# Kernel tuning notes

Hardware: AMD Instinct MI355X
Metric: run time of the kernel (lower is better)

Reference implementation:

```python
import jax, jax.numpy as jnp
import numpy as np

W = 32        # local_context
M = 128       # nb_features
TEMP = 1.0    # softmax_temp
NEG = -1e24   # mask fill used by local_dot_product in the original


def _log_features(x, proj):
    # Performer softmax-kernel log-features (before stabilization).
    # x: (B,H,N,E), proj: (M,E) -> (B,H,N,M); exp(q.k*TEMP) ~ (1/M) sum_m phi_q phi_k
    xn = x * np.float32(np.sqrt(TEMP))
    d = jnp.einsum('bhne,me->bhnm', xn, proj)
    diag = 0.5 * jnp.sum(xn * xn, axis=-1, keepdims=True)
    return d - diag


def _sb_local_chunk(q, k, v, proj):
    # Scatterbrain SBLocalAttention: exact softmax scores inside a centered local
    # window of size W, Performer low-rank approximation outside, shared normalizer.
    # q: (B,H,L,E) chunk queries; k,v: (B,H,S,E); proj: (M,E)
    B, H, L, E = q.shape
    S = k.shape[2]
    nb, half = L // W, W // 2

    logq = _log_features(q, proj)
    stab_q = jax.lax.stop_gradient(jnp.max(logq, axis=-1, keepdims=True))        # per-query stabilizer
    phi_q = jnp.exp(logq - stab_q)
    logk = _log_features(k, proj)
    stab_k = jax.lax.stop_gradient(jnp.max(logk, axis=(-1, -2), keepdims=True))  # global key stabilizer
    phi_k = jnp.exp(logk - stab_k)
    # true low-rank score = (phi_q . phi_k) * exp(prime_log_scale)
    pls = stab_q[..., 0] + stab_k[..., 0] - np.float32(np.log(M))                # (B,H,L)

    # Low-rank (linear attention) sums over ALL keys
    kv = jnp.einsum('bhsm,bhsd->bhmd', phi_k, v)
    lr_v = jnp.einsum('bhlm,bhmd->bhld', phi_q, kv)            # (B,H,L,E)
    lr_1 = jnp.einsum('bhlm,bhm->bhl', phi_q, phi_k.sum(2))    # (B,H,L)

    # Local window: query position t attends keys [t-W//2, t+W//2).
    # Gather 3 key blocks of size W per query block instead of per-query windows.
    q_blk = q.reshape(B, H, nb, W, E)
    phiq_blk = phi_q.reshape(B, H, nb, W, M)
    idx3 = W * jnp.arange(nb)[:, None] + jnp.arange(3 * W)[None, :]   # (nb,3W) into padded seq
    pad = [(0, 0), (0, 0), (W, W), (0, 0)]
    k3 = jnp.pad(k, pad)[:, :, idx3]          # (B,H,nb,3W,E)
    v3 = jnp.pad(v, pad)[:, :, idx3]
    phik3 = jnp.pad(phi_k, pad)[:, :, idx3]   # (B,H,nb,3W,M)

    pos = idx3[:, None, :] - W                # absolute key positions (nb,1,3W)
    rel = pos - (W * jnp.arange(nb)[:, None, None] + jnp.arange(W)[None, :, None])
    mask = (rel >= -half) & (rel < half) & (pos >= 0) & (pos < S)     # (nb,W,3W)

    scores = TEMP * jnp.einsum('bhnqe,bhnke->bhnqk', q_blk, k3)
    scores = jnp.where(mask, scores, NEG)
    dots_p = jnp.where(mask, jnp.einsum('bhnqm,bhnkm->bhnqk', phiq_blk, phik3), 0.0)

    qk_lse = jax.nn.logsumexp(scores, axis=-1).reshape(B, H, L)
    # low-rank mass minus the in-window part it double counts (>= 0 since phi >= 0)
    lr_rem = jnp.clip(lr_1 - dots_p.sum(-1).reshape(B, H, L), 1e-24, None)
    log_norm = jnp.logaddexp(qk_lse, jnp.log(lr_rem) + pls)           # (B,H,L)

    p_local = jnp.exp(scores - log_norm.reshape(B, H, nb, W, 1))
    out_local = jnp.einsum('bhnqk,bhnke->bhnqe', p_local, v3).reshape(B, H, L, E)
    lr_v_win = jnp.einsum('bhnqk,bhnke->bhnqe', dots_p, v3).reshape(B, H, L, E)
    return out_local + (lr_v - lr_v_win) * jnp.exp(pls - log_norm)[..., None]


def _forward(query, key, value, proj):
    # query/key/value: (B,T,H,E) as in the torch module; proj: (4,M,E), one random
    # feature matrix per chunk (module builds a fresh SBLocalAttention each chunk).
    q = jnp.transpose(query, (0, 2, 1, 3))
    k = jnp.transpose(key, (0, 2, 1, 3))
    v = jnp.transpose(value, (0, 2, 1, 3))
    B, H, T, E = q.shape
    CH = 1024
    qc = q.reshape(B, H, T // CH, CH, E).transpose(2, 0, 1, 3, 4)     # (4,B,H,CH,E)
    outs = jax.vmap(_sb_local_chunk, in_axes=(0, None, None, 0))(qc, k, v, proj)
    # torch.cat(att, 1).transpose(1, 2) -> (B,H,T,E)
    return outs.transpose(1, 2, 0, 3, 4).reshape(B, H, T, E)


def setup_inputs() -> dict:
    key = jax.random.key(0)
    k1, k2, k3, k4 = jax.random.split(key, 4)
    B, T, S, H, E = 4, 4096, 4096, 8, 64
    return {
        'query': jax.random.normal(k1, (B, T, H, E), dtype=jnp.float32),
        'key': jax.random.normal(k2, (B, S, H, E), dtype=jnp.float32),
        'value': jax.random.normal(k3, (B, S, H, E), dtype=jnp.float32),
        'proj': jax.random.normal(k4, (4, M, E), dtype=jnp.float32),
    }


def reference(query, key, value, proj):
    return _forward(query, key, value, proj)
```

## Files before the change

### kernel.cpp

```cpp
#include <hip/hip_runtime.h>

typedef unsigned short u16;
typedef unsigned int   u32;
typedef __attribute__((ext_vector_type(8))) short short8;
typedef __attribute__((ext_vector_type(4))) float f32x4;

#define LOGM 4.852030263919617f

constexpr int WS_PMAX = 0;
constexpr int WS_K1   = 2048;
constexpr int WS_KV   = 18432;
constexpr int WS_PHIK = 1067008;
constexpr int WS_PLS  = 9717760;
constexpr int WS_LR1  = 9848832;
constexpr int WS_PHIQ = 9979904;
constexpr int WS_LRV  = 18368512;

__device__ __forceinline__ float b2f(u16 u){ union { u32 i; float f; } x; x.i = ((u32)u) << 16; return x.f; }
__device__ __forceinline__ u16 f2b(float f){ union { float f; u32 i; } x; x.f = f; return (u16)((x.i + 0x7fffu + ((x.i >> 16) & 1u)) >> 16); }

__global__ __launch_bounds__(256, 2) void k_phi(const float* __restrict__ key,
                                                const float* __restrict__ val,
                                                const float* __restrict__ proj,
                                                float* __restrict__ ws){
  __shared__ __align__(16) u16 phit[128*72];
  __shared__ __align__(16) u16 vt[64*72];
  __shared__ float sred[4];
  const int tid = threadIdx.x;
  const int wave = tid >> 6, l = tid & 63;
  const int g = l >> 4, r16 = l & 15;
  const int kq = blockIdx.x, combo = blockIdx.y;
  const int c = combo >> 5, b = (combo >> 3) & 3, h = combo & 7;
  const float* projc = proj + c*8192;

  {
    const float4* pr = (const float4*)(projc + (tid & 127)*64);
    float pn = 0.f;
    #pragma unroll
    for(int i=0;i<16;i++){ float4 u = pr[i]; pn = fmaf(u.x,u.x,fmaf(u.y,u.y,fmaf(u.z,u.z,fmaf(u.w,u.w,pn)))); }
    #pragma unroll
    for(int o=1;o<64;o<<=1) pn = fmaxf(pn, __shfl_xor(pn, o));
    if(l == 0) sred[wave] = pn;
  }
  __syncthreads();
  const float stab = 0.5f * fmaxf(fmaxf(sred[0],sred[1]), fmaxf(sred[2],sred[3]));
  if(kq == 0 && tid == 0) ws[WS_PMAX + combo] = stab;

  short8 ph[8][2], pl[8][2];
  #pragma unroll
  for(int mt=0;mt<8;mt++){
    #pragma unroll
    for(int ks=0;ks<2;ks++){
      const float* pb = projc + (mt*16 + r16)*64 + ks*32 + g*8;
      float4 u0 = *(const float4*)pb;
      float4 u1 = *(const float4*)(pb + 4);
      float x[8] = {u0.x,u0.y,u0.z,u0.w,u1.x,u1.y,u1.z,u1.w};
      #pragma unroll
      for(int j=0;j<8;j++){
        u16 hb = f2b(x[j]);
        ph[mt][ks][j] = (short)hb;
        pl[mt][ks][j] = (short)f2b(x[j] - b2f(hb));
      }
    }
  }

  const f32x4 zero4 = {0.f,0.f,0.f,0.f};
  f32x4 kvacc[2][4];
  #pragma unroll
  for(int i=0;i<2;i++)
    #pragma unroll
    for(int j=0;j<4;j++) kvacc[i][j] = zero4;
  float k1p0 = 0.f, k1p1 = 0.f;
  u16* phikg = ((u16*)(ws + WS_PHIK)) + (size_t)combo*1056*128;

  for(int t0=0;t0<16;t0++){
    const int s_tile = kq*1024 + t0*64;
    const int sA = s_tile + wave*16 + r16;
    const float* krow = key + (size_t)(b*4096 + sA)*512 + h*64;
    float areg[16];
    #pragma unroll
    for(int ks=0;ks<2;ks++){
      float4 u0 = *(const float4*)(krow + ks*32 + g*8);
      float4 u1 = *(const float4*)(krow + ks*32 + g*8 + 4);
      areg[ks*8+0]=u0.x; areg[ks*8+1]=u0.y; areg[ks*8+2]=u0.z; areg[ks*8+3]=u0.w;
      areg[ks*8+4]=u1.x; areg[ks*8+5]=u1.y; areg[ks*8+6]=u1.z; areg[ks*8+7]=u1.w;
    }
    float ksq = 0.f;
    #pragma unroll
    for(int e=0;e<16;e++) ksq = fmaf(areg[e], areg[e], ksq);
    ksq += __shfl_xor(ksq, 16);
    ksq += __shfl_xor(ksq, 32);
    ksq *= 0.5f;
    short8 ah[2], al[2];
    #pragma unroll
    for(int ks=0;ks<2;ks++){
      #pragma unroll
      for(int j=0;j<8;j++){
        float x = areg[ks*8+j];
        u16 hb = f2b(x);
        ah[ks][j] = (short)hb;
        al[ks][j] = (short)f2b(x - b2f(hb));
      }
    }
    f32x4 acc[8];
    #pragma unroll
    for(int mt=0;mt<8;mt++) acc[mt] = zero4;
    #pragma unroll
    for(int ks=0;ks<2;ks++){
      #pragma unroll
      for(int mt=0;mt<8;mt++){
        acc[mt] = __builtin_amdgcn_mfma_f32_16x16x32_bf16(ah[ks], ph[mt][ks], acc[mt], 0, 0, 0);
        acc[mt] = __builtin_amdgcn_mfma_f32_16x16x32_bf16(ah[ks], pl[mt][ks], acc[mt], 0, 0, 0);
        acc[mt] = __builtin_amdgcn_mfma_f32_16x16x32_bf16(al[ks], ph[mt][ks], acc[mt], 0, 0, 0);
      }
    }
    const float kc0 = __shfl(ksq, 4*g + 0);
    const float kc1 = __shfl(ksq, 4*g + 1);
    const float kc2 = __shfl(ksq, 4*g + 2);
    const float kc3 = __shfl(ksq, 4*g + 3);
    #pragma unroll
    for(int mt=0;mt<8;mt++){
      ushort4 pw;
      pw.x = f2b(__expf(acc[mt][0] - kc0 - stab));
      pw.y = f2b(__expf(acc[mt][1] - kc1 - stab));
      pw.z = f2b(__expf(acc[mt][2] - kc2 - stab));
      pw.w = f2b(__expf(acc[mt][3] - kc3 - stab));
      *(ushort4*)(phit + (mt*16 + r16)*72 + wave*16 + 4*g) = pw;
    }
    __syncthreads();
    if(s_tile < 1056){
      const int m = tid & 127, kh = tid >> 7;
      for(int kk=0;kk<32;kk++){
        int skey = kh*32 + kk, gs = s_tile + skey;
        if(gs < 1056) phikg[(size_t)gs*128 + m] = phit[m*72 + skey];
      }
    }
    #pragma unroll
    for(int i=0;i<4;i++){
      int flat = tid + 256*i;
      int sv = flat >> 4, d4 = (flat & 15)*4;
      const float4 u = *(const float4*)(val + (size_t)(b*4096 + s_tile + sv)*512 + h*64 + d4);
      vt[(d4+0)*72 + sv] = f2b(u.x);
      vt[(d4+1)*72 + sv] = f2b(u.y);
      vt[(d4+2)*72 + sv] = f2b(u.z);
      vt[(d4+3)*72 + sv] = f2b(u.w);
    }
    __syncthreads();
    #pragma unroll
    for(int ks=0;ks<2;ks++){
      short8 af0 = *(const short8*)(phit + ((2*wave+0)*16 + r16)*72 + ks*32 + g*8);
      short8 af1 = *(const short8*)(phit + ((2*wave+1)*16 + r16)*72 + ks*32 + g*8);
      short8 bf[4];
      #pragma unroll
      for(int dt=0;dt<4;dt++) bf[dt] = *(const short8*)(vt + (dt*16 + r16)*72 + ks*32 + g*8);
      #pragma unroll
      for(int dt=0;dt<4;dt++){
        kvacc[0][dt] = __builtin_amdgcn_mfma_f32_16x16x32_bf16(af0, bf[dt], kvacc[0][dt], 0, 0, 0);
        kvacc[1][dt] = __builtin_amdgcn_mfma_f32_16x16x32_bf16(af1, bf[dt], kvacc[1][dt], 0, 0, 0);
      }
      #pragma unroll
      for(int j=0;j<8;j++){ k1p0 += b2f((u16)af0[j]); k1p1 += b2f((u16)af1[j]); }
    }
    __syncthreads();
  }
  k1p0 += __shfl_xor(k1p0, 16); k1p0 += __shfl_xor(k1p0, 32);
  k1p1 += __shfl_xor(k1p1, 16); k1p1 += __shfl_xor(k1p1, 32);
  if(l < 16){
    atomicAdd(ws + WS_K1 + combo*128 + (2*wave+0)*16 + l, k1p0);
    atomicAdd(ws + WS_K1 + combo*128 + (2*wave+1)*16 + l, k1p1);
  }
  #pragma unroll
  for(int mi=0;mi<2;mi++){
    #pragma unroll
    for(int dt=0;dt<4;dt++){
      #pragma unroll
      for(int rr=0;rr<4;rr++){
        int m = (2*wave+mi)*16 + 4*g + rr;
        int d = dt*16 + r16;
        atomicAdd(ws + WS_KV + (size_t)combo*8192 + m*64 + d, kvacc[mi][dt][rr]);
      }
    }
  }
}

__global__ __launch_bounds__(256, 2) void k_q(const float* __restrict__ qry,
                                              const float* __restrict__ proj,
                                              float* __restrict__ ws){
  __shared__ __align__(16) u16 phiqs[64*136];
  __shared__ __align__(16) u16 kvt[64*136];
  __shared__ float k1s[128];
  const int tid = threadIdx.x;
  const int wave = tid >> 6, l = tid & 63;
  const int g = l >> 4, r16 = l & 15;
  const int qt = blockIdx.x, combo = blockIdx.y;
  const int c = combo >> 5, b = (combo >> 3) & 3, h = combo & 7;
  const float* projc = proj + c*8192;
  const float stab = ws[WS_PMAX + combo];
  if(tid < 128) k1s[tid] = ws[WS_K1 + combo*128 + tid];
  const float* kvg = ws + WS_KV + (size_t)combo*8192;
  #pragma unroll
  for(int i=0;i<8;i++){
    int flat = tid + 256*i;
    int m = flat >> 4, d4 = (flat & 15)*4;
    float4 u = *(const float4*)(kvg + m*64 + d4);
    kvt[(d4+0)*136 + m] = f2b(u.x);
    kvt[(d4+1)*136 + m] = f2b(u.y);
    kvt[(d4+2)*136 + m] = f2b(u.z);
    kvt[(d4+3)*136 + m] = f2b(u.w);
  }
  const int qrow = qt*64 + wave*16 + r16;
  const float* qr = qry + (size_t)(b*4096 + (c*1024 + qrow))*512 + h*64;
  float areg[16];
  #pragma unroll
  for(int ks=0;ks<2;ks++){
    float4 u0 = *(const float4*)(qr + ks*32 + g*8);
    float4 u1 = *(const float4*)(qr + ks*32 + g*8 + 4);
    areg[ks*8+0]=u0.x; areg[ks*8+1]=u0.y; areg[ks*8+2]=u0.z; areg[ks*8+3]=u0.w;
    areg[ks*8+4]=u1.x; areg[ks*8+5]=u1.y; areg[ks*8+6]=u1.z; areg[ks*8+7]=u1.w;
  }
  float qsq = 0.f;
  #pragma unroll
  for(int e=0;e<16;e++) qsq = fmaf(areg[e], areg[e], qsq);
  qsq += __shfl_xor(qsq, 16);
  qsq += __shfl_xor(qsq, 32);
  qsq *= 0.5f;
  short8 ah[2], al[2];
  #pragma unroll
  for(int ks=0;ks<2;ks++){
    #pragma unroll
    for(int j=0;j<8;j++){
      float x = areg[ks*8+j];
      u16 hb = f2b(x);
      ah[ks][j] = (short)hb;
      al[ks][j] = (short)f2b(x - b2f(hb));
    }
  }
  const f32x4 zero4 = {0.f,0.f,0.f,0.f};
  f32x4 acc[8];
  #pragma unroll
  for(int mt=0;mt<8;mt++) acc[mt] = zero4;
  #pragma unroll
  for(int ks=0;ks<2;ks++){
    #pragma unroll
    for(int mt=0;mt<8;mt++){
      const float* pb = projc + (mt*16 + r16)*64 + ks*32 + g*8;
      float4 u0 = *(const float4*)pb;
      float4 u1 = *(const float4*)(pb + 4);
      float x[8] = {u0.x,u0.y,u0.z,u0.w,u1.x,u1.y,u1.z,u1.w};
      short8 pph, ppl;
      #pragma unroll
      for(int j=0;j<8;j++){
        u16 hb = f2b(x[j]);
        pph[j] = (short)hb;
        ppl[j] = (short)f2b(x[j] - b2f(hb));
      }
      acc[mt] = __builtin_amdgcn_mfma_f32_16x16x32_bf16(ah[ks], pph, acc[mt], 0, 0, 0);
      acc[mt] = __builtin_amdgcn_mfma_f32_16x16x32_bf16(ah[ks], ppl, acc[mt], 0, 0, 0);
      acc[mt] = __builtin_amdgcn_mfma_f32_16x16x32_bf16(al[ks], pph, acc[mt], 0, 0, 0);
    }
  }
  float qsr[4];
  #pragma unroll
  for(int r=0;r<4;r++) qsr[r] = __shfl(qsq, 4*g + r);
  float amax[4];
  #pragma unroll
  for(int r=0;r<4;r++){
    float m = -3e38f;
    #pragma unroll
    for(int mt=0;mt<8;mt++) m = fmaxf(m, acc[mt][r]);
    m = fmaxf(m, __shfl_xor(m, 1));
    m = fmaxf(m, __shfl_xor(m, 2));
    m = fmaxf(m, __shfl_xor(m, 4));
    m = fmaxf(m, __shfl_xor(m, 8));
    amax[r] = m;
  }
  float lrp[4] = {0.f,0.f,0.f,0.f};
  #pragma unroll
  for(int mt=0;mt<8;mt++){
    const float k1v = k1s[mt*16 + r16];
    #pragma unroll
    for(int r=0;r<4;r++){
      float phv = __expf(acc[mt][r] - amax[r]);
      phiqs[(wave*16 + 4*g + r)*136 + mt*16 + r16] = f2b(phv);
      lrp[r] = fmaf(phv, k1v, lrp[r]);
    }
  }
  #pragma unroll
  for(int r=0;r<4;r++){
    lrp[r] += __shfl_xor(lrp[r], 1);
    lrp[r] += __shfl_xor(lrp[r], 2);
    lrp[r] += __shfl_xor(lrp[r], 4);
    lrp[r] += __shfl_xor(lrp[r], 8);
  }
  if(r16 == 0){
    #pragma unroll
    for(int r=0;r<4;r++){
      int row = qt*64 + wave*16 + 4*g + r;
      ws[WS_PLS + combo*1024 + row] = amax[r] - qsr[r] + stab - LOGM;
      ws[WS_LR1 + combo*1024 + row] = lrp[r];
    }
  }
  __syncthreads();
  f32x4 lacc[4];
  #pragma unroll
  for(int dt=0;dt<4;dt++) lacc[dt] = zero4;
  #pragma unroll
  for(int ks=0;ks<4;ks++){
    short8 a = *(const short8*)(phiqs + (wave*16 + r16)*136 + ks*32 + g*8);
    #pragma unroll
    for(int dt=0;dt<4;dt++){
      short8 bfr = *(const short8*)(kvt + (dt*16 + r16)*136 + ks*32 + g*8);
      lacc[dt] = __builtin_amdgcn_mfma_f32_16x16x32_bf16(a, bfr, lacc[dt], 0, 0, 0);
    }
  }
  u16* lrvg = ((u16*)(ws + WS_LRV)) + ((size_t)combo*1024 + qt*64)*64;
  #pragma unroll
  for(int dt=0;dt<4;dt++){
    #pragma unroll
    for(int r=0;r<4;r++)
      lrvg[(wave*16 + 4*g + r)*64 + dt*16 + r16] = f2b(lacc[dt][r]);
  }
  u16* phiqg = ((u16*)(ws + WS_PHIQ)) + ((size_t)combo*1024 + qt*64)*128;
  #pragma unroll
  for(int i=0;i<8;i++){
    int flat = tid + 256*i;
    int row = flat >> 5, c4 = (flat & 31)*4;
    *(ushort4*)(phiqg + flat*4) = *(const ushort4*)(phiqs + row*136 + c4);
  }
}

__global__ __launch_bounds__(256, 2) void k_main(const float* __restrict__ qry,
                                                 const float* __restrict__ key,
                                                 const float* __restrict__ val,
                                                 float* __restrict__ ws,
                                                 float* __restrict__ out){
  __shared__ __align__(16) u16 buf[30720];
  u16* khs  = buf;
  u16* kls  = buf + 6912;
  u16* phik = buf + 13824;
  u16* cjh  = buf;
  u16* cjl  = buf + 8704;
  u16* vt   = buf + 17408;
  u16* vtl  = buf + 24064;

  const int tid = threadIdx.x;
  const int wave = tid >> 6, l = tid & 63;
  const int g = l >> 4, r16 = l & 15;
  const int qt = blockIdx.x, combo = blockIdx.y;
  const int c = combo >> 5, b = (combo >> 3) & 3, h = combo & 7;
  const int s_base = qt*64 - 16;

  const u16* phikg = ((const u16*)(ws + WS_PHIK)) + (size_t)combo*1056*128;
  float4 vreg[6];
  #pragma unroll
  for(int i=0;i<6;i++){
    int flat = tid + 256*i;
    int j = flat >> 4, e4 = (flat & 15)*4;
    int s = s_base + j;
    float4 u = {0.f,0.f,0.f,0.f};
    float4 w4 = {0.f,0.f,0.f,0.f};
    if(s >= 0){
      u  = *(const float4*)(key + (((size_t)b*4096 + s)*8 + h)*64 + e4);
      w4 = *(const float4*)(val + (((size_t)b*4096 + s)*8 + h)*64 + e4);
    }
    vreg[i] = w4;
    ushort4 hh, ll;
    hh.x = f2b(u.x); ll.x = f2b(u.x - b2f(hh.x));
    hh.y = f2b(u.y); ll.y = f2b(u.y - b2f(hh.y));
    hh.z = f2b(u.z); ll.z = f2b(u.z - b2f(hh.z));
    hh.w = f2b(u.w); ll.w = f2b(u.w - b2f(hh.w));
    *(ushort4*)(khs + j*72 + e4) = hh;
    *(ushort4*)(kls + j*72 + e4) = ll;
  }
  #pragma unroll
  for(int i=0;i<12;i++){
    int flat = tid + 256*i;
    int j = flat >> 5, c4 = (flat & 31)*4;
    int s = s_base + j;
    ushort4 p = {0,0,0,0};
    if(s >= 0) p = *(const ushort4*)(phikg + (size_t)s*128 + c4);
    *(ushort4*)(phik + j*136 + c4) = p;
  }
  const int qrow = qt*64 + wave*16 + r16;
  const float* qr = qry + (((size_t)b*4096 + (c*1024 + qrow))*8 + h)*64;
  short8 ah[2], al[2];
  #pragma unroll
  for(int ks=0;ks<2;ks++){
    float4 u0 = *(const float4*)(qr + ks*32 + g*8);
    float4 u1 = *(const float4*)(qr + ks*32 + g*8 + 4);
    float x[8] = {u0.x,u0.y,u0.z,u0.w,u1.x,u1.y,u1.z,u1.w};
    #pragma unroll
    for(int jj=0;jj<8;jj++){
      u16 hb = f2b(x[jj]);
      ah[ks][jj] = (short)hb;
      al[ks][jj] = (short)f2b(x[jj] - b2f(hb));
    }
  }
  const u16* phiqg = ((const u16*)(ws + WS_PHIQ)) + ((size_t)combo*1024 + qt*64)*128;
  short8 pa[4];
  #pragma unroll
  for(int ks=0;ks<4;ks++)
    pa[ks] = *(const short8*)(phiqg + (wave*16 + r16)*128 + ks*32 + g*8);
  float plsr[4], lr1r[4];
  #pragma unroll
  for(int r=0;r<4;r++){
    int row = qt*64 + wave*16 + 4*g + r;
    plsr[r] = ws[WS_PLS + combo*1024 + row];
    lr1r[r] = ws[WS_LR1 + combo*1024 + row];
  }
  __syncthreads();

  const f32x4 zero4 = {0.f,0.f,0.f,0.f};
  f32x4 sacc[6], dacc[6];
  #pragma unroll
  for(int j=0;j<6;j++){ sacc[j] = zero4; dacc[j] = zero4; }
  #pragma unroll
  for(int j=0;j<6;j++){
    #pragma unroll
    for(int ks=0;ks<2;ks++){
      short8 kbh = *(const short8*)(khs + (j*16 + r16)*72 + ks*32 + g*8);
      short8 kbl = *(const short8*)(kls + (j*16 + r16)*72 + ks*32 + g*8);
      sacc[j] = __builtin_amdgcn_mfma_f32_16x16x32_bf16(ah[ks], kbh, sacc[j], 0, 0, 0);
      sacc[j] = __builtin_amdgcn_mfma_f32_16x16x32_bf16(al[ks], kbh, sacc[j], 0, 0, 0);
      sacc[j] = __builtin_amdgcn_mfma_f32_16x16x32_bf16(ah[ks], kbl, sacc[j], 0, 0, 0);
    }
    #pragma unroll
    for(int ks=0;ks<4;ks++){
      short8 pb = *(const short8*)(phik + (j*16 + r16)*136 + ks*32 + g*8);
      dacc[j] = __builtin_amdgcn_mfma_f32_16x16x32_bf16(pa[ks], pb, dacc[j], 0, 0, 0);
    }
  }
  __syncthreads();

  #pragma unroll
  for(int i=0;i<6;i++){
    int flat = tid + 256*i;
    int j = flat >> 4, e4 = (flat & 15)*4;
    float4 u = vreg[i];
    u16 h0 = f2b(u.x), h1 = f2b(u.y), h2 = f2b(u.z), h3 = f2b(u.w);
    vt[(e4+0)*104 + j] = h0; vtl[(e4+0)*104 + j] = f2b(u.x - b2f(h0));
    vt[(e4+1)*104 + j] = h1; vtl[(e4+1)*104 + j] = f2b(u.y - b2f(h1));
    vt[(e4+2)*104 + j] = h2; vtl[(e4+2)*104 + j] = f2b(u.z - b2f(h2));
    vt[(e4+3)*104 + j] = h3; vtl[(e4+3)*104 + j] = f2b(u.w - b2f(h3));
  }
  const int rowb = wave*16 + 4*g;
  float m1r[4] = {-1e30f,-1e30f,-1e30f,-1e30f};
  #pragma unroll
  for(int j=0;j<6;j++){
    #pragma unroll
    for(int r=0;r<4;r++){
      int rel = 16*j + r16 - 16 - (rowb + r);
      bool ok = (rel >= -16) && (rel < 16) && (s_base + 16*j + r16 >= 0);
      if(ok) m1r[r] = fmaxf(m1r[r], sacc[j][r]);
    }
  }
  #pragma unroll
  for(int r=0;r<4;r++){
    m1r[r] = fmaxf(m1r[r], __shfl_xor(m1r[r], 1));
    m1r[r] = fmaxf(m1r[r], __shfl_xor(m1r[r], 2));
    m1r[r] = fmaxf(m1r[r], __shfl_xor(m1r[r], 4));
    m1r[r] = fmaxf(m1r[r], __shfl_xor(m1r[r], 8));
  }
  float ser[4] = {0.f,0.f,0.f,0.f}, wpr[4] = {0.f,0.f,0.f,0.f};
  #pragma unroll
  for(int j=0;j<6;j++){
    #pragma unroll
    for(int r=0;r<4;r++){
      int rel = 16*j + r16 - 16 - (rowb + r);
      bool ok = (rel >= -16) && (rel < 16) && (s_base + 16*j + r16 >= 0);
      if(ok){
        ser[r] += __expf(sacc[j][r] - m1r[r]);
        wpr[r] += dacc[j][r];
      }
    }
  }
  #pragma unroll
  for(int r=0;r<4;r++){
    ser[r] += __shfl_xor(ser[r], 1); ser[r] += __shfl_xor(ser[r], 2);
    ser[r] += __shfl_xor(ser[r], 4); ser[r] += __shfl_xor(ser[r], 8);
    wpr[r] += __shfl_xor(wpr[r], 1); wpr[r] += __shfl_xor(wpr[r], 2);
    wpr[r] += __shfl_xor(wpr[r], 4); wpr[r] += __shfl_xor(wpr[r], 8);
  }
  float lnr[4], scr[4];
  #pragma unroll
  for(int r=0;r<4;r++){
    float qk_lse = m1r[r] + __logf(ser[r]);
    float lrem = fmaxf(lr1r[r] - wpr[r], 1e-37f);
    float bb = __logf(lrem) + plsr[r];
    float ln = fmaxf(qk_lse, bb) + log1pf(__expf(-fabsf(qk_lse - bb)));
    lnr[r] = ln;
    scr[r] = __expf(plsr[r] - ln);
  }
  #pragma unroll
  for(int j=0;j<6;j++){
    #pragma unroll
    for(int r=0;r<4;r++){
      int rel = 16*j + r16 - 16 - (rowb + r);
      bool ok = (rel >= -16) && (rel < 16) && (s_base + 16*j + r16 >= 0);
      float cj = ok ? (__expf(sacc[j][r] - lnr[r]) - scr[r]*dacc[j][r]) : 0.f;
      u16 hb = f2b(cj);
      cjh[(rowb + r)*136 + 16*j + r16] = hb;
      cjl[(rowb + r)*136 + 16*j + r16] = f2b(cj - b2f(hb));
    }
  }
  __syncthreads();

  f32x4 oacc[4];
  #pragma unroll
  for(int dt=0;dt<4;dt++) oacc[dt] = zero4;
  #pragma unroll
  for(int ks=0;ks<3;ks++){
    short8 ch = *(const short8*)(cjh + (wave*16 + r16)*136 + ks*32 + g*8);
    short8 cl = *(const short8*)(cjl + (wave*16 + r16)*136 + ks*32 + g*8);
    #pragma unroll
    for(int dt=0;dt<4;dt++){
      short8 vbh = *(const short8*)(vt  + (dt*16 + r16)*104 + ks*32 + g*8);
      short8 vbl = *(const short8*)(vtl + (dt*16 + r16)*104 + ks*32 + g*8);
      oacc[dt] = __builtin_amdgcn_mfma_f32_16x16x32_bf16(ch, vbh, oacc[dt], 0, 0, 0);
      oacc[dt] = __builtin_amdgcn_mfma_f32_16x16x32_bf16(cl, vbh, oacc[dt], 0, 0, 0);
      oacc[dt] = __builtin_amdgcn_mfma_f32_16x16x32_bf16(ch, vbl, oacc[dt], 0, 0, 0);
    }
  }
  const u16* lrvg = ((const u16*)(ws + WS_LRV)) + ((size_t)combo*1024 + qt*64)*64;
  #pragma unroll
  for(int r=0;r<4;r++){
    int row = rowb + r;
    float* ob = out + ((((size_t)b*8 + h)*4096) + (size_t)c*1024 + qt*64 + row)*64;
    #pragma unroll
    for(int dt=0;dt<4;dt++){
      float lv = b2f(lrvg[row*64 + dt*16 + r16]);
      ob[dt*16 + r16] = oacc[dt][r] + scr[r]*lv;
    }
  }
}

extern "C" void kernel_launch(void* const* d_in, const int* in_sizes, int n_in,
                              void* d_out, int out_size, void* d_ws, size_t ws_size,
                              hipStream_t stream){
  (void)in_sizes; (void)n_in; (void)out_size; (void)ws_size;
  const float* q = (const float*)d_in[0];
  const float* k = (const float*)d_in[1];
  const float* v = (const float*)d_in[2];
  const float* p = (const float*)d_in[3];
  float* out = (float*)d_out;
  float* ws = (float*)d_ws;
  hipMemsetAsync(ws + WS_K1, 0, (size_t)(16384 + 1048576)*sizeof(float), stream);
  k_phi <<<dim3(4,128),  256, 0, stream>>>(k, v, p, ws);
  k_q   <<<dim3(16,128), 256, 0, stream>>>(q, p, ws);
  k_main<<<dim3(16,128), 256, 0, stream>>>(q, k, v, ws, out);
}
```

Measured before the change: 370.2 us.

## Split key phase across more blocks with partial buffers and a reduction kernel

The key-feature kernel now uses 8 blocks per head/chunk over 512 keys each instead of 4 over 1024, doubling the grid. Per-block KV and key-sum partials go to separate workspace slots, and a new reduction kernel sums them, replacing the global atomics and the memset. The phi_k store for the first 1056 keys now goes through an LDS transpose buffer and vectorised row writes instead of scalar strided stores. This adds an extra kernel launch and extra partial-buffer traffic. It also reuses the phi_q and lr_v workspace regions as scratch before the later kernels overwrite them.

```diff
diff --git a/kernel.cpp b/kernel.cpp
--- a/kernel.cpp
+++ b/kernel.cpp
@@ -15,6 +15,8 @@
 constexpr int WS_LR1  = 9848832;
 constexpr int WS_PHIQ = 9979904;
 constexpr int WS_LRV  = 18368512;
+constexpr int WS_KVP  = WS_PHIQ;
+constexpr int WS_K1P  = WS_LRV;
 
 __device__ __forceinline__ float b2f(u16 u){ union { u32 i; float f; } x; x.i = ((u32)u) << 16; return x.f; }
 __device__ __forceinline__ u16 f2b(float f){ union { float f; u32 i; } x; x.f = f; return (u16)((x.i + 0x7fffu + ((x.i >> 16) & 1u)) >> 16); }
@@ -24,8 +26,10 @@
                                                 const float* __restrict__ proj,
                                                 float* __restrict__ ws){
   __shared__ __align__(16) u16 phit[128*72];
-  __shared__ __align__(16) u16 vt[64*72];
+  __shared__ __align__(16) u16 buf2[8704];
   __shared__ float sred[4];
+  u16* vt = buf2;
+  u16* phit2 = buf2;
   const int tid = threadIdx.x;
   const int wave = tid >> 6, l = tid & 63;
   const int g = l >> 4, r16 = l & 15;
@@ -73,8 +77,9 @@
   float k1p0 = 0.f, k1p1 = 0.f;
   u16* phikg = ((u16*)(ws + WS_PHIK)) + (size_t)combo*1056*128;
 
-  for(int t0=0;t0<16;t0++){
-    const int s_tile = kq*1024 + t0*64;
+  for(int t0=0;t0<8;t0++){
+    const int s_tile = kq*512 + t0*64;
+    const bool dtile = (s_tile < 1056);
     const int sA = s_tile + wave*16 + r16;
     const float* krow = key + (size_t)(b*4096 + sA)*512 + h*64;
     float areg[16];
@@ -126,14 +131,25 @@
       pw.z = f2b(__expf(acc[mt][2] - kc2 - stab));
       pw.w = f2b(__expf(acc[mt][3] - kc3 - stab));
       *(ushort4*)(phit + (mt*16 + r16)*72 + wave*16 + 4*g) = pw;
+      if(dtile){
+        u16* p2 = phit2 + (wave*16 + 4*g)*132 + mt*16 + r16;
+        p2[0*132] = pw.x;
+        p2[1*132] = pw.y;
+        p2[2*132] = pw.z;
+        p2[3*132] = pw.w;
+      }
     }
     __syncthreads();
-    if(s_tile < 1056){
-      const int m = tid & 127, kh = tid >> 7;
-      for(int kk=0;kk<32;kk++){
-        int skey = kh*32 + kk, gs = s_tile + skey;
-        if(gs < 1056) phikg[(size_t)gs*128 + m] = phit[m*72 + skey];
-      }
+    if(dtile){
+      #pragma unroll
+      for(int i=0;i<8;i++){
+        int flat = tid + 256*i;
+        int row = flat >> 5, c4 = (flat & 31)*4;
+        int gs = s_tile + row;
+        if(gs < 1056)
+          *(ushort4*)(phikg + (size_t)gs*128 + c4) = *(const ushort4*)(phit2 + row*132 + c4);
+      }
+      __syncthreads();
     }
     #pragma unroll
     for(int i=0;i<4;i++){
@@ -166,9 +182,10 @@
   k1p0 += __shfl_xor(k1p0, 16); k1p0 += __shfl_xor(k1p0, 32);
   k1p1 += __shfl_xor(k1p1, 16); k1p1 += __shfl_xor(k1p1, 32);
   if(l < 16){
-    atomicAdd(ws + WS_K1 + combo*128 + (2*wave+0)*16 + l, k1p0);
-    atomicAdd(ws + WS_K1 + combo*128 + (2*wave+1)*16 + l, k1p1);
-  }
+    ws[WS_K1P + kq*16384 + combo*128 + (2*wave+0)*16 + l] = k1p0;
+    ws[WS_K1P + kq*16384 + combo*128 + (2*wave+1)*16 + l] = k1p1;
+  }
+  float* kvp = ws + WS_KVP + (size_t)kq*1048576 + (size_t)combo*8192;
   #pragma unroll
   for(int mi=0;mi<2;mi++){
     #pragma unroll
@@ -177,9 +194,31 @@
       for(int rr=0;rr<4;rr++){
         int m = (2*wave+mi)*16 + 4*g + rr;
         int d = dt*16 + r16;
-        atomicAdd(ws + WS_KV + (size_t)combo*8192 + m*64 + d, kvacc[mi][dt][rr]);
-      }
-    }
+        kvp[m*64 + d] = kvacc[mi][dt][rr];
+      }
+    }
+  }
+}
+
+__global__ __launch_bounds__(256) void k_red(float* __restrict__ ws){
+  const int i = blockIdx.x*256 + threadIdx.x;
+  const float* src = ws + WS_KVP + (size_t)i*4;
+  float4 s = {0.f,0.f,0.f,0.f};
+  #pragma unroll
+  for(int p=0;p<8;p++){
+    float4 u = *(const float4*)(src + (size_t)p*1048576);
+    s.x += u.x; s.y += u.y; s.z += u.z; s.w += u.w;
+  }
+  *(float4*)(ws + WS_KV + (size_t)i*4) = s;
+  if(blockIdx.x < 16){
+    const int j = blockIdx.x*256 + threadIdx.x;
+    float4 t = {0.f,0.f,0.f,0.f};
+    #pragma unroll
+    for(int p=0;p<8;p++){
+      float4 u = *(const float4*)(ws + WS_K1P + p*16384 + j*4);
+      t.x += u.x; t.y += u.y; t.z += u.z; t.w += u.w;
+    }
+    *(float4*)(ws + WS_K1 + j*4) = t;
   }
 }
 
@@ -544,8 +583,8 @@
   const float* p = (const float*)d_in[3];
   float* out = (float*)d_out;
   float* ws = (float*)d_ws;
-  hipMemsetAsync(ws + WS_K1, 0, (size_t)(16384 + 1048576)*sizeof(float), stream);
-  k_phi <<<dim3(4,128),  256, 0, stream>>>(k, v, p, ws);
+  k_phi <<<dim3(8,128),  256, 0, stream>>>(k, v, p, ws);
+  k_red <<<dim3(1024),   256, 0, stream>>>(ws);
   k_q   <<<dim3(16,128), 256, 0, stream>>>(q, p, ws);
   k_main<<<dim3(16,128), 256, 0, stream>>>(q, k, v, ws, out);
 }
```

After: 409.7 us. 1.11x slower.

## Split k_phi over more blocks, prefetch values, swizzle LDS, write phi_k directly

Applied to the files above, without the earlier changes.

Doubles the k_phi grid so each block processes 512 keys instead of 1024, which raises parallelism from 512 to 1024 blocks. Value loads are issued early into registers so they overlap the feature MFMA work. The transposed value tile in LDS uses an XOR swizzle to cut bank conflicts. The phi_k slice for the first 1056 keys is now written straight from registers, which removes a sync and a serial copy loop. More blocks also means more atomicAdd contention on the shared KV and k1 accumulators.

```diff
diff --git a/kernel.cpp b/kernel.cpp
--- a/kernel.cpp
+++ b/kernel.cpp
@@ -73,8 +73,9 @@
   float k1p0 = 0.f, k1p1 = 0.f;
   u16* phikg = ((u16*)(ws + WS_PHIK)) + (size_t)combo*1056*128;
 
-  for(int t0=0;t0<16;t0++){
-    const int s_tile = kq*1024 + t0*64;
+  for(int t0=0;t0<8;t0++){
+    const int s_tile = kq*512 + t0*64;
+    const bool dtile = (s_tile < 1056);
     const int sA = s_tile + wave*16 + r16;
     const float* krow = key + (size_t)(b*4096 + sA)*512 + h*64;
     float areg[16];
@@ -85,6 +86,13 @@
       areg[ks*8+0]=u0.x; areg[ks*8+1]=u0.y; areg[ks*8+2]=u0.z; areg[ks*8+3]=u0.w;
       areg[ks*8+4]=u1.x; areg[ks*8+5]=u1.y; areg[ks*8+6]=u1.z; areg[ks*8+7]=u1.w;
     }
+    float4 vreg[4];
+    #pragma unroll
+    for(int i=0;i<4;i++){
+      int flat = tid + 256*i;
+      int sv = flat >> 4, d4 = (flat & 15)*4;
+      vreg[i] = *(const float4*)(val + (size_t)(b*4096 + s_tile + sv)*512 + h*64 + d4);
+    }
     float ksq = 0.f;
     #pragma unroll
     for(int e=0;e<16;e++) ksq = fmaf(areg[e], areg[e], ksq);
@@ -118,6 +126,7 @@
     const float kc1 = __shfl(ksq, 4*g + 1);
     const float kc2 = __shfl(ksq, 4*g + 2);
     const float kc3 = __shfl(ksq, 4*g + 3);
+    const int gs = s_tile + wave*16 + r16;
     #pragma unroll
     for(int mt=0;mt<8;mt++){
       ushort4 pw;
@@ -126,24 +135,19 @@
       pw.z = f2b(__expf(acc[mt][2] - kc2 - stab));
       pw.w = f2b(__expf(acc[mt][3] - kc3 - stab));
       *(ushort4*)(phit + (mt*16 + r16)*72 + wave*16 + 4*g) = pw;
-    }
-    __syncthreads();
-    if(s_tile < 1056){
-      const int m = tid & 127, kh = tid >> 7;
-      for(int kk=0;kk<32;kk++){
-        int skey = kh*32 + kk, gs = s_tile + skey;
-        if(gs < 1056) phikg[(size_t)gs*128 + m] = phit[m*72 + skey];
-      }
+      if(dtile && gs < 1056)
+        *(ushort4*)(phikg + (size_t)gs*128 + mt*16 + 4*g) = pw;
     }
     #pragma unroll
     for(int i=0;i<4;i++){
       int flat = tid + 256*i;
       int sv = flat >> 4, d4 = (flat & 15)*4;
-      const float4 u = *(const float4*)(val + (size_t)(b*4096 + s_tile + sv)*512 + h*64 + d4);
-      vt[(d4+0)*72 + sv] = f2b(u.x);
-      vt[(d4+1)*72 + sv] = f2b(u.y);
-      vt[(d4+2)*72 + sv] = f2b(u.z);
-      vt[(d4+3)*72 + sv] = f2b(u.w);
+      float x[4] = {vreg[i].x, vreg[i].y, vreg[i].z, vreg[i].w};
+      #pragma unroll
+      for(int j=0;j<4;j++){
+        int d = d4 + j;
+        vt[d*72 + (sv ^ (8*((d>>2)&7)))] = f2b(x[j]);
+      }
     }
     __syncthreads();
     #pragma unroll
@@ -152,7 +156,11 @@
       short8 af1 = *(const short8*)(phit + ((2*wave+1)*16 + r16)*72 + ks*32 + g*8);
       short8 bf[4];
       #pragma unroll
-      for(int dt=0;dt<4;dt++) bf[dt] = *(const short8*)(vt + (dt*16 + r16)*72 + ks*32 + g*8);
+      for(int dt=0;dt<4;dt++){
+        int d = dt*16 + r16;
+        int col = (ks*32 + g*8) ^ (8*((d>>2)&7));
+        bf[dt] = *(const short8*)(vt + d*72 + col);
+      }
       #pragma unroll
       for(int dt=0;dt<4;dt++){
         kvacc[0][dt] = __builtin_amdgcn_mfma_f32_16x16x32_bf16(af0, bf[dt], kvacc[0][dt], 0, 0, 0);
@@ -545,7 +553,7 @@
   float* out = (float*)d_out;
   float* ws = (float*)d_ws;
   hipMemsetAsync(ws + WS_K1, 0, (size_t)(16384 + 1048576)*sizeof(float), stream);
-  k_phi <<<dim3(4,128),  256, 0, stream>>>(k, v, p, ws);
+  k_phi <<<dim3(8,128),  256, 0, stream>>>(k, v, p, ws);
   k_q   <<<dim3(16,128), 256, 0, stream>>>(q, p, ws);
   k_main<<<dim3(16,128), 256, 0, stream>>>(q, k, v, ws, out);
 }
```

New measurement: 408.2 us. 10.2% more time.

## Double-buffer phi/V tiles in k_phi, prefetch keys, swizzle V LDS

Applied to the files above, without the earlier changes.

Restructures the k_phi tile loop to use double-buffered LDS for phi and V, which removes one of the two barriers per tile. Key rows for the next tile are prefetched into registers, and value loads are issued early. The phi_k global write now goes straight from registers instead of through a serial LDS copy loop. V is stored transposed with an XOR swizzle to cut LDS bank conflicts. Register pressure goes up, which may hurt occupancy under the 2-blocks launch bound.

```diff
diff --git a/kernel.cpp b/kernel.cpp
--- a/kernel.cpp
+++ b/kernel.cpp
@@ -23,8 +23,8 @@
                                                 const float* __restrict__ val,
                                                 const float* __restrict__ proj,
                                                 float* __restrict__ ws){
-  __shared__ __align__(16) u16 phit[128*72];
-  __shared__ __align__(16) u16 vt[64*72];
+  __shared__ __align__(16) u16 phit[2][128*72];
+  __shared__ __align__(16) u16 vt[2][64*72];
   __shared__ float sred[4];
   const int tid = threadIdx.x;
   const int wave = tid >> 6, l = tid & 63;
@@ -32,6 +32,15 @@
   const int kq = blockIdx.x, combo = blockIdx.y;
   const int c = combo >> 5, b = (combo >> 3) & 3, h = combo & 7;
   const float* projc = proj + c*8192;
+
+  float4 ka[4], kb[4];
+  {
+    const float* krow0 = key + (size_t)(b*4096 + kq*1024 + wave*16 + r16)*512 + h*64;
+    ka[0] = *(const float4*)(krow0 + g*8);
+    ka[1] = *(const float4*)(krow0 + g*8 + 4);
+    ka[2] = *(const float4*)(krow0 + 32 + g*8);
+    ka[3] = *(const float4*)(krow0 + 32 + g*8 + 4);
+  }
 
   {
     const float4* pr = (const float4*)(projc + (tid & 127)*64);
@@ -73,96 +82,108 @@
   float k1p0 = 0.f, k1p1 = 0.f;
   u16* phikg = ((u16*)(ws + WS_PHIK)) + (size_t)combo*1056*128;
 
-  for(int t0=0;t0<16;t0++){
-    const int s_tile = kq*1024 + t0*64;
-    const int sA = s_tile + wave*16 + r16;
-    const float* krow = key + (size_t)(b*4096 + sA)*512 + h*64;
-    float areg[16];
-    #pragma unroll
-    for(int ks=0;ks<2;ks++){
-      float4 u0 = *(const float4*)(krow + ks*32 + g*8);
-      float4 u1 = *(const float4*)(krow + ks*32 + g*8 + 4);
-      areg[ks*8+0]=u0.x; areg[ks*8+1]=u0.y; areg[ks*8+2]=u0.z; areg[ks*8+3]=u0.w;
-      areg[ks*8+4]=u1.x; areg[ks*8+5]=u1.y; areg[ks*8+6]=u1.z; areg[ks*8+7]=u1.w;
-    }
-    float ksq = 0.f;
-    #pragma unroll
-    for(int e=0;e<16;e++) ksq = fmaf(areg[e], areg[e], ksq);
-    ksq += __shfl_xor(ksq, 16);
-    ksq += __shfl_xor(ksq, 32);
-    ksq *= 0.5f;
-    short8 ah[2], al[2];
-    #pragma unroll
-    for(int ks=0;ks<2;ks++){
-      #pragma unroll
-      for(int j=0;j<8;j++){
-        float x = areg[ks*8+j];
-        u16 hb = f2b(x);
-        ah[ks][j] = (short)hb;
-        al[ks][j] = (short)f2b(x - b2f(hb));
-      }
-    }
-    f32x4 acc[8];
-    #pragma unroll
-    for(int mt=0;mt<8;mt++) acc[mt] = zero4;
-    #pragma unroll
-    for(int ks=0;ks<2;ks++){
-      #pragma unroll
-      for(int mt=0;mt<8;mt++){
-        acc[mt] = __builtin_amdgcn_mfma_f32_16x16x32_bf16(ah[ks], ph[mt][ks], acc[mt], 0, 0, 0);
-        acc[mt] = __builtin_amdgcn_mfma_f32_16x16x32_bf16(ah[ks], pl[mt][ks], acc[mt], 0, 0, 0);
-        acc[mt] = __builtin_amdgcn_mfma_f32_16x16x32_bf16(al[ks], ph[mt][ks], acc[mt], 0, 0, 0);
-      }
-    }
-    const float kc0 = __shfl(ksq, 4*g + 0);
-    const float kc1 = __shfl(ksq, 4*g + 1);
-    const float kc2 = __shfl(ksq, 4*g + 2);
-    const float kc3 = __shfl(ksq, 4*g + 3);
-    #pragma unroll
-    for(int mt=0;mt<8;mt++){
-      ushort4 pw;
-      pw.x = f2b(__expf(acc[mt][0] - kc0 - stab));
-      pw.y = f2b(__expf(acc[mt][1] - kc1 - stab));
-      pw.z = f2b(__expf(acc[mt][2] - kc2 - stab));
-      pw.w = f2b(__expf(acc[mt][3] - kc3 - stab));
-      *(ushort4*)(phit + (mt*16 + r16)*72 + wave*16 + 4*g) = pw;
-    }
-    __syncthreads();
-    if(s_tile < 1056){
-      const int m = tid & 127, kh = tid >> 7;
-      for(int kk=0;kk<32;kk++){
-        int skey = kh*32 + kk, gs = s_tile + skey;
-        if(gs < 1056) phikg[(size_t)gs*128 + m] = phit[m*72 + skey];
-      }
-    }
-    #pragma unroll
-    for(int i=0;i<4;i++){
-      int flat = tid + 256*i;
-      int sv = flat >> 4, d4 = (flat & 15)*4;
-      const float4 u = *(const float4*)(val + (size_t)(b*4096 + s_tile + sv)*512 + h*64 + d4);
-      vt[(d4+0)*72 + sv] = f2b(u.x);
-      vt[(d4+1)*72 + sv] = f2b(u.y);
-      vt[(d4+2)*72 + sv] = f2b(u.z);
-      vt[(d4+3)*72 + sv] = f2b(u.w);
-    }
-    __syncthreads();
-    #pragma unroll
-    for(int ks=0;ks<2;ks++){
-      short8 af0 = *(const short8*)(phit + ((2*wave+0)*16 + r16)*72 + ks*32 + g*8);
-      short8 af1 = *(const short8*)(phit + ((2*wave+1)*16 + r16)*72 + ks*32 + g*8);
-      short8 bf[4];
-      #pragma unroll
-      for(int dt=0;dt<4;dt++) bf[dt] = *(const short8*)(vt + (dt*16 + r16)*72 + ks*32 + g*8);
-      #pragma unroll
-      for(int dt=0;dt<4;dt++){
-        kvacc[0][dt] = __builtin_amdgcn_mfma_f32_16x16x32_bf16(af0, bf[dt], kvacc[0][dt], 0, 0, 0);
-        kvacc[1][dt] = __builtin_amdgcn_mfma_f32_16x16x32_bf16(af1, bf[dt], kvacc[1][dt], 0, 0, 0);
-      }
-      #pragma unroll
-      for(int j=0;j<8;j++){ k1p0 += b2f((u16)af0[j]); k1p1 += b2f((u16)af1[j]); }
-    }
-    __syncthreads();
-  }
+#define PHI_TILE(T0, KC, KN, PB)                                                          \
+{                                                                                          \
+  const int s_tile = kq*1024 + (T0)*64;                                                    \
+  const bool dtile = (s_tile < 1056);                                                      \
+  if((T0) < 15){                                                                           \
+    const float* krow2 = key + (size_t)(b*4096 + s_tile + 64 + wave*16 + r16)*512 + h*64;  \
+    KN[0] = *(const float4*)(krow2 + g*8);                                                 \
+    KN[1] = *(const float4*)(krow2 + g*8 + 4);                                             \
+    KN[2] = *(const float4*)(krow2 + 32 + g*8);                                            \
+    KN[3] = *(const float4*)(krow2 + 32 + g*8 + 4);                                        \
+  }                                                                                        \
+  float4 vreg[4];                                                                          \
+  _Pragma("unroll")                                                                        \
+  for(int i=0;i<4;i++){                                                                    \
+    int flat = tid + 256*i;                                                                \
+    int sv = flat >> 4, d4 = (flat & 15)*4;                                                \
+    vreg[i] = *(const float4*)(val + (size_t)(b*4096 + s_tile + sv)*512 + h*64 + d4);      \
+  }                                                                                        \
+  float areg[16] = {KC[0].x,KC[0].y,KC[0].z,KC[0].w, KC[1].x,KC[1].y,KC[1].z,KC[1].w,      \
+                    KC[2].x,KC[2].y,KC[2].z,KC[2].w, KC[3].x,KC[3].y,KC[3].z,KC[3].w};     \
+  float ksq = 0.f;                                                                         \
+  _Pragma("unroll")                                                                        \
+  for(int e=0;e<16;e++) ksq = fmaf(areg[e], areg[e], ksq);                                 \
+  ksq += __shfl_xor(ksq, 16); ksq += __shfl_xor(ksq, 32); ksq *= 0.5f;                     \
+  short8 ah[2], al[2];                                                                     \
+  _Pragma("unroll")                                                                        \
+  for(int ks=0;ks<2;ks++){                                                                 \
+    _Pragma("unroll")                                                                      \
+    for(int j=0;j<8;j++){                                                                  \
+      float x = areg[ks*8+j];                                                              \
+      u16 hb = f2b(x);                                                                     \
+      ah[ks][j] = (short)hb;                                                               \
+      al[ks][j] = (short)f2b(x - b2f(hb));                                                 \
+    }                                                                                      \
+  }                                                                                        \
+  f32x4 acc[8];                                                                            \
+  _Pragma("unroll")                                                                        \
+  for(int mt=0;mt<8;mt++) acc[mt] = zero4;                                                 \
+  _Pragma("unroll")                                                                        \
+  for(int ks=0;ks<2;ks++){                                                                 \
+    _Pragma("unroll")                                                                      \
+    for(int mt=0;mt<8;mt++){                                                               \
+      acc[mt] = __builtin_amdgcn_mfma_f32_16x16x32_bf16(ah[ks], ph[mt][ks], acc[mt],0,0,0);\
+      acc[mt] = __builtin_amdgcn_mfma_f32_16x16x32_bf16(ah[ks], pl[mt][ks], acc[mt],0,0,0);\
+      acc[mt] = __builtin_amdgcn_mfma_f32_16x16x32_bf16(al[ks], ph[mt][ks], acc[mt],0,0,0);\
+    }                                                                                      \
+  }                                                                                        \
+  const float kc0 = __shfl(ksq, 4*g + 0);                                                  \
+  const float kc1 = __shfl(ksq, 4*g + 1);                                                  \
+  const float kc2 = __shfl(ksq, 4*g + 2);                                                  \
+  const float kc3 = __shfl(ksq, 4*g + 3);                                                  \
+  const int gs = s_tile + wave*16 + r16;                                                   \
+  _Pragma("unroll")                                                                        \
+  for(int mt=0;mt<8;mt++){                                                                 \
+    ushort4 pw;                                                                            \
+    pw.x = f2b(__expf(acc[mt][0] - kc0 - stab));                                           \
+    pw.y = f2b(__expf(acc[mt][1] - kc1 - stab));                                           \
+    pw.z = f2b(__expf(acc[mt][2] - kc2 - stab));                                           \
+    pw.w = f2b(__expf(acc[mt][3] - kc3 - stab));                                           \
+    *(ushort4*)(phit[PB] + (mt*16 + r16)*72 + wave*16 + 4*g) = pw;                         \
+    if(dtile && gs < 1056)                                                                 \
+      *(ushort4*)(phikg + (size_t)gs*128 + mt*16 + 4*g) = pw;                              \
+  }                                                                                        \
+  _Pragma("unroll")                                                                        \
+  for(int i=0;i<4;i++){                                                                    \
+    int flat = tid + 256*i;                                                                \
+    int sv = flat >> 4, d4 = (flat & 15)*4;                                                \
+    float xx[4] = {vreg[i].x, vreg[i].y, vreg[i].z, vreg[i].w};                            \
+    _Pragma("unroll")                                                                      \
+    for(int j=0;j<4;j++){                                                                  \
+      int d = d4 + j;                                                                      \
+      vt[PB][d*72 + (sv ^ (8*((d>>2)&7)))] = f2b(xx[j]);                                   \
+    }                                                                                      \
+  }                                                                                        \
+  __syncthreads();                                                                         \
+  _Pragma("unroll")                                                                        \
+  for(int ks=0;ks<2;ks++){                                                                 \
+    short8 af0 = *(const short8*)(phit[PB] + ((2*wave+0)*16 + r16)*72 + ks*32 + g*8);      \
+    short8 af1 = *(const short8*)(phit[PB] + ((2*wave+1)*16 + r16)*72 + ks*32 + g*8);      \
+    short8 bfv[4];                                                                         \
+    _Pragma("unroll")                                                                      \
+    for(int dt=0;dt<4;dt++){                                                               \
+      int d = dt*16 + r16;                                                                 \
+      int col = (ks*32 + g*8) ^ (8*((d>>2)&7));                                            \
+      bfv[dt] = *(const short8*)(vt[PB] + d*72 + col);                                     \
+    }                                                                                      \
+    _Pragma("unroll")                                                                      \
+    for(int dt=0;dt<4;dt++){                                                               \
+      kvacc[0][dt] = __builtin_amdgcn_mfma_f32_16x16x32_bf16(af0, bfv[dt], kvacc[0][dt],0,0,0); \
+      kvacc[1][dt] = __builtin_amdgcn_mfma_f32_16x16x32_bf16(af1, bfv[dt], kvacc[1][dt],0,0,0); \
+    }                                                                                      \
+    _Pragma("unroll")                                                                      \
+    for(int j=0;j<8;j++){ k1p0 += b2f((u16)af0[j]); k1p1 += b2f((u16)af1[j]); }            \
+  }                                                                                        \
+}
+
+  for(int tt=0; tt<16; tt+=2){
+    PHI_TILE(tt,   ka, kb, 0)
+    PHI_TILE(tt+1, kb, ka, 1)
+  }
+#undef PHI_TILE
+
   k1p0 += __shfl_xor(k1p0, 16); k1p0 += __shfl_xor(k1p0, 32);
   k1p1 += __shfl_xor(k1p1, 16); k1p1 += __shfl_xor(k1p1, 32);
   if(l < 16){
```

Result: slower. 395.1 us (+6.7%).
